# Kernel tuning notes

Hardware: AMD Instinct MI355X
Metric: run time of the kernel (lower is better)

Reference implementation:

```python
import jax, jax.numpy as jnp
import numpy as np

B, T, E, H = 512, 256, 384, 64

def setup_inputs() -> dict:
    key = jax.random.key(0)
    k1, k2, k3, k4 = jax.random.split(key, 4)
    scale = 1.0 / np.sqrt(E)
    return {
        "x":  jax.random.normal(k1, (B, T, E), dtype=jnp.float32),
        "Wq": jax.random.normal(k2, (E, H), dtype=jnp.float32) * scale,
        "Wk": jax.random.normal(k3, (E, H), dtype=jnp.float32) * scale,
        "Wv": jax.random.normal(k4, (E, H), dtype=jnp.float32) * scale,
    }

def reference(x, Wq, Wk, Wv):
    # single-head causal self-attention (dropout in eval mode / identity)
    q = jnp.einsum('bte,eh->bth', x, Wq)
    k = jnp.einsum('bte,eh->bth', x, Wk)
    v = jnp.einsum('bte,eh->bth', x, Wv)
    d = q.shape[-1]
    wei = jnp.einsum('bqh,bkh->bqk', q, k) * (d ** -0.5)   # [B,T,T]
    T_ = x.shape[1]
    causal = jnp.tril(jnp.ones((T_, T_), dtype=bool))
    wei = jnp.where(causal[None, :, :], wei, -jnp.inf)
    wei = jax.nn.softmax(wei, axis=-1)
    out = jnp.einsum('bqk,bkh->bqh', wei, v)               # [B,T,H]
    return out
```

## Files before the change

### kernel.cpp

```cpp
#include <hip/hip_runtime.h>

typedef __attribute__((ext_vector_type(4)))  float f32x4;
typedef __attribute__((ext_vector_type(16))) float f32x16;
typedef __attribute__((ext_vector_type(8)))  short s16x8;
typedef __attribute__((ext_vector_type(4)))  short s16x4;


__device__ inline short f2bf(float f){
  unsigned u = __float_as_uint(f);
  u = u + 0x7fffu + ((u >> 16) & 1u);
  return (short)(u >> 16);
}

__global__ void wt_prep_kernel(const float* __restrict__ Wq, const float* __restrict__ Wk,
                               const float* __restrict__ Wv, short* __restrict__ Wt){
  int o = blockIdx.x * 256 + threadIdx.x;
  if (o >= 192*384) return;
  int n = o / 384, k = o - n*384;
  const float* W = (n < 64) ? Wq : (n < 128) ? Wk : Wv;
  Wt[o] = f2bf(W[k*64 + (n & 63)]);
}

__global__ __launch_bounds__(512, 2) void fused_kernel(const float* __restrict__ x,
                             const short* __restrict__ Wt, float* __restrict__ out){
  __shared__ __align__(16) short Qs[256*72];
  __shared__ __align__(16) short Ks[256*72];
  __shared__ __align__(16) short Vts[64*264];
  __shared__ __align__(16) short Pp[8][16*40];

  const int tid  = threadIdx.x;
  const int w    = tid >> 6, lane = tid & 63;
  const int l31  = lane & 31, hh = lane >> 5;
  const int b    = blockIdx.x;

  const float* xb = x + ((long)b*256 + w*32)*384;

  f32x16 acc[6];
  #pragma unroll
  for (int c = 0; c < 6; ++c)
    #pragma unroll
    for (int j = 0; j < 16; ++j) acc[c][j] = 0.0f;

  #pragma unroll 2
  for (int kt = 0; kt < 6; ++kt){
    #pragma unroll
    for (int s = 0; s < 4; ++s){
      const int k0 = kt*64 + s*16 + hh*8;
      const float* xp = xb + l31*384 + k0;
      float4 a0 = *(const float4*)xp;
      float4 a1 = *(const float4*)(xp + 4);
      s16x8 bx;
      bx[0]=f2bf(a0.x); bx[1]=f2bf(a0.y); bx[2]=f2bf(a0.z); bx[3]=f2bf(a0.w);
      bx[4]=f2bf(a1.x); bx[5]=f2bf(a1.y); bx[6]=f2bf(a1.z); bx[7]=f2bf(a1.w);
      #pragma unroll
      for (int c = 0; c < 6; ++c){
        s16x8 wa = *(const s16x8*)(Wt + (c*32 + l31)*384 + k0);
        acc[c] = __builtin_amdgcn_mfma_f32_32x32x16_bf16(wa, bx, acc[c], 0, 0, 0);
      }
    }
  }

  const int trow = w*32 + l31;
  #pragma unroll
  for (int c = 0; c < 4; ++c){
    short* dst = (c < 2) ? Qs : Ks;
    const int nb = (c & 1)*32;
    #pragma unroll
    for (int g = 0; g < 4; ++g){
      s16x4 v;
      #pragma unroll
      for (int i = 0; i < 4; ++i) v[i] = f2bf(acc[c][g*4 + i]);
      *(s16x4*)(dst + trow*72 + nb + 8*g + 4*hh) = v;
    }
  }
  #pragma unroll
  for (int c = 4; c < 6; ++c)
    #pragma unroll
    for (int reg = 0; reg < 16; ++reg){
      const int h = (c-4)*32 + (reg & 3) + 8*(reg >> 2) + 4*hh;
      Vts[h*264 + trow] = f2bf(acc[c][reg]);
    }

  __syncthreads();

  const int l15 = lane & 15, quad = lane >> 4;
  float* ob = out + (long)b*256*64;
  short* Pw = Pp[w];

  for (int it = 0; it < 2; ++it){
    const int F  = it ? (15 - w) : w;
    const int qb = F*16;
    const int NF = F + 1;
    const int NS = (NF + 1) >> 1;

    s16x8 qf0 = *(const s16x8*)(Qs + (qb + l15)*72 + quad*8);
    s16x8 qf1 = *(const s16x8*)(Qs + (qb + l15)*72 + 32 + quad*8);

    f32x4 sc[16];
    #pragma unroll
    for (int f = 0; f < 16; ++f){
      f32x4 a;
      #pragma unroll
      for (int r = 0; r < 4; ++r) a[r] = 0.0f;
      if (f < NF){
        const short* kp = Ks + (f*16 + l15)*72 + quad*8;
        s16x8 k0v = *(const s16x8*)kp;
        s16x8 k1v = *(const s16x8*)(kp + 32);
        a = __builtin_amdgcn_mfma_f32_16x16x32_bf16(qf0, k0v, a, 0, 0, 0);
        a = __builtin_amdgcn_mfma_f32_16x16x32_bf16(qf1, k1v, a, 0, 0, 0);
      }
      sc[f] = a;
    }

    float mx[4], sm[4];
    #pragma unroll
    for (int r = 0; r < 4; ++r) mx[r] = -3.0e38f;
    #pragma unroll
    for (int f = 0; f < 16; ++f){
      if (f < NF){
        const int key = f*16 + l15;
        #pragma unroll
        for (int r = 0; r < 4; ++r){
          const int qg = qb + quad*4 + r;
          float s = sc[f][r] * 0.125f;
          s = (key <= qg) ? s : -1.0e30f;
          sc[f][r] = s;
          mx[r] = fmaxf(mx[r], s);
        }
      }
    }
    #pragma unroll
    for (int r = 0; r < 4; ++r){
      #pragma unroll
      for (int off = 1; off < 16; off <<= 1) mx[r] = fmaxf(mx[r], __shfl_xor(mx[r], off, 16));
    }
    #pragma unroll
    for (int r = 0; r < 4; ++r) sm[r] = 0.0f;
    #pragma unroll
    for (int f = 0; f < 16; ++f){
      if (f < NF){
        #pragma unroll
        for (int r = 0; r < 4; ++r){
          float p = exp2f((sc[f][r] - mx[r]) * 1.44269504f);
          sc[f][r] = p;
          sm[r] += p;
        }
      }
    }
    #pragma unroll
    for (int r = 0; r < 4; ++r){
      #pragma unroll
      for (int off = 1; off < 16; off <<= 1) sm[r] += __shfl_xor(sm[r], off, 16);
    }

    f32x4 o[4];
    #pragma unroll
    for (int h0 = 0; h0 < 4; ++h0)
      #pragma unroll
      for (int r = 0; r < 4; ++r) o[h0][r] = 0.0f;

    #pragma unroll
    for (int ks = 0; ks < 8; ++ks){
      if (ks < NS){
        #pragma unroll
        for (int fi = 0; fi < 2; ++fi){
          const int f = 2*ks + fi;
          #pragma unroll
          for (int r = 0; r < 4; ++r){
            short v = 0;
            if (f < NF) v = f2bf(sc[f][r]);
            Pw[(quad*4 + r)*40 + fi*16 + l15] = v;
          }
        }
        s16x8 pf = *(const s16x8*)(Pw + l15*40 + quad*8);
        #pragma unroll
        for (int h0 = 0; h0 < 4; ++h0){
          s16x8 vf = *(const s16x8*)(Vts + (h0*16 + l15)*264 + ks*32 + quad*8);
          o[h0] = __builtin_amdgcn_mfma_f32_16x16x32_bf16(pf, vf, o[h0], 0, 0, 0);
        }
      }
    }

    #pragma unroll
    for (int r = 0; r < 4; ++r){
      const float inv = 1.0f / sm[r];
      #pragma unroll
      for (int h0 = 0; h0 < 4; ++h0)
        ob[(qb + quad*4 + r)*64 + h0*16 + l15] = o[h0][r] * inv;
    }
  }
}

extern "C" void kernel_launch(void* const* d_in, const int* in_sizes, int n_in,
                              void* d_out, int out_size, void* d_ws, size_t ws_size,
                              hipStream_t stream){
  const float* x  = (const float*)d_in[0];
  const float* Wq = (const float*)d_in[1];
  const float* Wk = (const float*)d_in[2];
  const float* Wv = (const float*)d_in[3];
  float* out = (float*)d_out;

  short* Wt = (short*)d_ws;

  hipLaunchKernelGGL(wt_prep_kernel, dim3(288), dim3(256), 0, stream, Wq, Wk, Wv, Wt);
  hipLaunchKernelGGL(fused_kernel,   dim3(512), dim3(512), 0, stream, x, Wt, out);
}
```

Measured before the change: 363.0 us.

## Split fused attention into QKV projection and attention kernels via workspace

Replaces the single fused kernel with two kernels when the workspace is large enough. A QKV projection kernel writes bf16 Q, K and V^T to global memory with XOR-swizzled layouts, and an attention kernel loads K and V into LDS with global_load_lds and runs the causal softmax. The split lowers LDS and register pressure so each kernel can target 4 blocks per CU instead of 2. In exchange it adds about 48MB of global round-trip traffic and a second launch, and falls back to the fused kernel when the workspace is small.

```diff
diff --git a/kernel.cpp b/kernel.cpp
--- a/kernel.cpp
+++ b/kernel.cpp
@@ -10,6 +10,11 @@
   unsigned u = __float_as_uint(f);
   u = u + 0x7fffu + ((u >> 16) & 1u);
   return (short)(u >> 16);
+}
+
+__device__ __forceinline__ void gld16(const void* g, void* l){
+  __builtin_amdgcn_global_load_lds((const __attribute__((address_space(1))) void*)g,
+                                   (__attribute__((address_space(3))) void*)l, 16, 0, 0);
 }
 
 __global__ void wt_prep_kernel(const float* __restrict__ Wq, const float* __restrict__ Wk,
@@ -21,12 +26,229 @@
   Wt[o] = f2bf(W[k*64 + (n & 63)]);
 }
 
+__global__ __launch_bounds__(512, 4) void qkv_kernel(const float* __restrict__ x,
+    const short* __restrict__ Wt, short* __restrict__ Qg,
+    short* __restrict__ Kg, short* __restrict__ Vg){
+  const int tid  = threadIdx.x;
+  const int w    = tid >> 6, lane = tid & 63;
+  const int l15  = lane & 15, quad = lane >> 4;
+  const int b    = blockIdx.x;
+
+  const float* xb = x + (long)b*256*384;
+  short* Qb = Qg + (long)b*16384;
+  char*  Kb = (char*)(Kg + (long)b*16384);
+  char*  Vb = (char*)(Vg + (long)b*16384);
+
+  #pragma unroll 1
+  for (int p = 0; p < 2; ++p){
+    const int r0 = w*32 + p*16;
+    const int tr = r0 + l15;
+
+    f32x4 aq[4], ak[4], av[4];
+    #pragma unroll
+    for (int c = 0; c < 4; ++c)
+      #pragma unroll
+      for (int i = 0; i < 4; ++i){ aq[c][i]=0.f; ak[c][i]=0.f; av[c][i]=0.f; }
+
+    const float* xr = xb + (long)tr*384;
+    #pragma unroll 2
+    for (int kt = 0; kt < 12; ++kt){
+      const int k0 = kt*32 + quad*8;
+      float4 a0 = *(const float4*)(xr + k0);
+      float4 a1 = *(const float4*)(xr + k0 + 4);
+      s16x8 bx;
+      bx[0]=f2bf(a0.x); bx[1]=f2bf(a0.y); bx[2]=f2bf(a0.z); bx[3]=f2bf(a0.w);
+      bx[4]=f2bf(a1.x); bx[5]=f2bf(a1.y); bx[6]=f2bf(a1.z); bx[7]=f2bf(a1.w);
+      #pragma unroll
+      for (int c = 0; c < 4; ++c){
+        s16x8 wq = *(const s16x8*)(Wt + (c*16 + l15)*384 + k0);
+        aq[c] = __builtin_amdgcn_mfma_f32_16x16x32_bf16(wq, bx, aq[c], 0, 0, 0);
+      }
+      #pragma unroll
+      for (int c = 0; c < 4; ++c){
+        s16x8 wk = *(const s16x8*)(Wt + ((c+4)*16 + l15)*384 + k0);
+        ak[c] = __builtin_amdgcn_mfma_f32_16x16x32_bf16(wk, bx, ak[c], 0, 0, 0);
+      }
+      #pragma unroll
+      for (int c = 0; c < 4; ++c){
+        s16x8 wv = *(const s16x8*)(Wt + ((c+8)*16 + l15)*384 + k0);
+        av[c] = __builtin_amdgcn_mfma_f32_16x16x32_bf16(bx, wv, av[c], 0, 0, 0);
+      }
+    }
+
+    #pragma unroll
+    for (int c = 0; c < 4; ++c){
+      s16x4 v;
+      #pragma unroll
+      for (int i = 0; i < 4; ++i) v[i] = f2bf(aq[c][i]);
+      *(s16x4*)(Qb + tr*64 + c*16 + quad*4) = v;
+    }
+    {
+      const int swz = (tr & 7) << 4;
+      #pragma unroll
+      for (int c = 0; c < 4; ++c){
+        s16x4 v;
+        #pragma unroll
+        for (int i = 0; i < 4; ++i) v[i] = f2bf(ak[c][i]);
+        *(s16x4*)(Kb + tr*128 + ((c*32 + quad*8) ^ swz)) = v;
+      }
+    }
+    #pragma unroll
+    for (int c = 0; c < 4; ++c){
+      const int h   = c*16 + l15;
+      const int swz = (h & 7) << 4;
+      s16x4 v;
+      #pragma unroll
+      for (int i = 0; i < 4; ++i) v[i] = f2bf(av[c][i]);
+      *(s16x4*)(Vb + h*512 + (((r0 + quad*4)*2) ^ swz)) = v;
+    }
+  }
+}
+
+__global__ __launch_bounds__(512, 4) void attn_kernel(const short* __restrict__ Qg,
+    const short* __restrict__ Kg, const short* __restrict__ Vg,
+    float* __restrict__ out){
+  __shared__ __align__(16) short Ks[16384];
+  __shared__ __align__(16) short Vts[16384];
+  __shared__ __align__(16) short Pp[8][16*40];
+
+  const int tid  = threadIdx.x;
+  const int w    = tid >> 6, lane = tid & 63;
+  const int l15  = lane & 15, quad = lane >> 4;
+  const int b    = blockIdx.x;
+
+  const short* Qb = Qg + (long)b*16384;
+  const int F0 = w, F1 = 15 - w;
+  s16x8 qA0 = *(const s16x8*)(Qb + (F0*16 + l15)*64 + quad*8);
+  s16x8 qA1 = *(const s16x8*)(Qb + (F0*16 + l15)*64 + 32 + quad*8);
+  s16x8 qB0 = *(const s16x8*)(Qb + (F1*16 + l15)*64 + quad*8);
+  s16x8 qB1 = *(const s16x8*)(Qb + (F1*16 + l15)*64 + 32 + quad*8);
+
+  const char* Kb = (const char*)(Kg + (long)b*16384);
+  const char* Vb = (const char*)(Vg + (long)b*16384);
+  {
+    const int base = w*4096;
+    #pragma unroll
+    for (int i = 0; i < 4; ++i){
+      gld16(Kb + base + i*1024 + lane*16, (char*)Ks  + base + i*1024);
+      gld16(Vb + base + i*1024 + lane*16, (char*)Vts + base + i*1024);
+    }
+  }
+  __syncthreads();
+
+  float* ob = out + (long)b*256*64;
+  short* Pw = Pp[w];
+  const int swz = (l15 & 7) << 4;
+
+  auto attend = [&](int F, s16x8 qf0, s16x8 qf1){
+    const int qb = F*16;
+    const int NF = F + 1;
+    const int NS = (NF + 1) >> 1;
+
+    f32x4 sc[16];
+    #pragma unroll
+    for (int f = 0; f < 16; ++f){
+      f32x4 a;
+      #pragma unroll
+      for (int r = 0; r < 4; ++r) a[r] = 0.0f;
+      if (f < NF){
+        const char* kp = (const char*)Ks + (f*16 + l15)*128;
+        s16x8 k0v = *(const s16x8*)(kp + ((quad*16)      ^ swz));
+        s16x8 k1v = *(const s16x8*)(kp + ((64 + quad*16) ^ swz));
+        a = __builtin_amdgcn_mfma_f32_16x16x32_bf16(qf0, k0v, a, 0, 0, 0);
+        a = __builtin_amdgcn_mfma_f32_16x16x32_bf16(qf1, k1v, a, 0, 0, 0);
+      }
+      sc[f] = a;
+    }
+
+    float mx[4], sm[4];
+    #pragma unroll
+    for (int r = 0; r < 4; ++r) mx[r] = -3.0e38f;
+    #pragma unroll
+    for (int f = 0; f < 16; ++f){
+      if (f < NF){
+        const int key = f*16 + l15;
+        #pragma unroll
+        for (int r = 0; r < 4; ++r){
+          const int qg = qb + quad*4 + r;
+          float s = sc[f][r] * 0.125f;
+          s = (key <= qg) ? s : -1.0e30f;
+          sc[f][r] = s;
+          mx[r] = fmaxf(mx[r], s);
+        }
+      }
+    }
+    #pragma unroll
+    for (int r = 0; r < 4; ++r){
+      #pragma unroll
+      for (int off = 1; off < 16; off <<= 1) mx[r] = fmaxf(mx[r], __shfl_xor(mx[r], off, 16));
+    }
+    #pragma unroll
+    for (int r = 0; r < 4; ++r) sm[r] = 0.0f;
+    #pragma unroll
+    for (int f = 0; f < 16; ++f){
+      if (f < NF){
+        #pragma unroll
+        for (int r = 0; r < 4; ++r){
+          float p = exp2f((sc[f][r] - mx[r]) * 1.44269504f);
+          sc[f][r] = p;
+          sm[r] += p;
+        }
+      }
+    }
+    #pragma unroll
+    for (int r = 0; r < 4; ++r){
+      #pragma unroll
+      for (int off = 1; off < 16; off <<= 1) sm[r] += __shfl_xor(sm[r], off, 16);
+    }
+
+    f32x4 o[4];
+    #pragma unroll
+    for (int h0 = 0; h0 < 4; ++h0)
+      #pragma unroll
+      for (int r = 0; r < 4; ++r) o[h0][r] = 0.0f;
+
+    #pragma unroll
+    for (int ks = 0; ks < 8; ++ks){
+      if (ks < NS){
+        #pragma unroll
+        for (int fi = 0; fi < 2; ++fi){
+          const int f = 2*ks + fi;
+          #pragma unroll
+          for (int r = 0; r < 4; ++r){
+            short v = 0;
+            if (f < NF) v = f2bf(sc[f][r]);
+            Pw[(quad*4 + r)*40 + fi*16 + l15] = v;
+          }
+        }
+        s16x8 pf = *(const s16x8*)(Pw + l15*40 + quad*8);
+        #pragma unroll
+        for (int h0 = 0; h0 < 4; ++h0){
+          const char* vp = (const char*)Vts + (h0*16 + l15)*512;
+          s16x8 vf = *(const s16x8*)(vp + ((ks*64 + quad*16) ^ swz));
+          o[h0] = __builtin_amdgcn_mfma_f32_16x16x32_bf16(pf, vf, o[h0], 0, 0, 0);
+        }
+      }
+    }
+
+    #pragma unroll
+    for (int r = 0; r < 4; ++r){
+      const float inv = 1.0f / sm[r];
+      #pragma unroll
+      for (int h0 = 0; h0 < 4; ++h0)
+        ob[(qb + quad*4 + r)*64 + h0*16 + l15] = o[h0][r] * inv;
+    }
+  };
+  attend(F0, qA0, qA1);
+  attend(F1, qB0, qB1);
+}
+
 __global__ __launch_bounds__(512, 2) void fused_kernel(const float* __restrict__ x,
                              const short* __restrict__ Wt, float* __restrict__ out){
   __shared__ __align__(16) short Qs[256*72];
-  __shared__ __align__(16) short Ks[256*72];
-  __shared__ __align__(16) short Vts[64*264];
-  __shared__ __align__(16) short Pp[8][16*40];
+  __shared__ __align__(16) short Ks2[256*72];
+  __shared__ __align__(16) short Vts2[64*264];
+  __shared__ __align__(16) short Pp2[8][16*40];
 
   const int tid  = threadIdx.x;
   const int w    = tid >> 6, lane = tid & 63;
@@ -63,7 +285,7 @@
   const int trow = w*32 + l31;
   #pragma unroll
   for (int c = 0; c < 4; ++c){
-    short* dst = (c < 2) ? Qs : Ks;
+    short* dst = (c < 2) ? Qs : Ks2;
     const int nb = (c & 1)*32;
     #pragma unroll
     for (int g = 0; g < 4; ++g){
@@ -78,14 +300,14 @@
     #pragma unroll
     for (int reg = 0; reg < 16; ++reg){
       const int h = (c-4)*32 + (reg & 3) + 8*(reg >> 2) + 4*hh;
-      Vts[h*264 + trow] = f2bf(acc[c][reg]);
+      Vts2[h*264 + trow] = f2bf(acc[c][reg]);
     }
 
   __syncthreads();
 
   const int l15 = lane & 15, quad = lane >> 4;
   float* ob = out + (long)b*256*64;
-  short* Pw = Pp[w];
+  short* Pw = Pp2[w];
 
   for (int it = 0; it < 2; ++it){
     const int F  = it ? (15 - w) : w;
@@ -103,7 +325,7 @@
       #pragma unroll
       for (int r = 0; r < 4; ++r) a[r] = 0.0f;
       if (f < NF){
-        const short* kp = Ks + (f*16 + l15)*72 + quad*8;
+        const short* kp = Ks2 + (f*16 + l15)*72 + quad*8;
         s16x8 k0v = *(const s16x8*)kp;
         s16x8 k1v = *(const s16x8*)(kp + 32);
         a = __builtin_amdgcn_mfma_f32_16x16x32_bf16(qf0, k0v, a, 0, 0, 0);
@@ -175,7 +397,7 @@
         s16x8 pf = *(const s16x8*)(Pw + l15*40 + quad*8);
         #pragma unroll
         for (int h0 = 0; h0 < 4; ++h0){
-          s16x8 vf = *(const s16x8*)(Vts + (h0*16 + l15)*264 + ks*32 + quad*8);
+          s16x8 vf = *(const s16x8*)(Vts2 + (h0*16 + l15)*264 + ks*32 + quad*8);
           o[h0] = __builtin_amdgcn_mfma_f32_16x16x32_bf16(pf, vf, o[h0], 0, 0, 0);
         }
       }
@@ -201,7 +423,16 @@
   float* out = (float*)d_out;
 
   short* Wt = (short*)d_ws;
+  const size_t need = 147456 + 3ull*16777216ull;
 
   hipLaunchKernelGGL(wt_prep_kernel, dim3(288), dim3(256), 0, stream, Wq, Wk, Wv, Wt);
-  hipLaunchKernelGGL(fused_kernel,   dim3(512), dim3(512), 0, stream, x, Wt, out);
-}
+  if (ws_size >= need){
+    short* Qg = (short*)((char*)d_ws + 147456);
+    short* Kg = Qg + 8388608;
+    short* Vg = Kg + 8388608;
+    hipLaunchKernelGGL(qkv_kernel,  dim3(512), dim3(512), 0, stream, x, Wt, Qg, Kg, Vg);
+    hipLaunchKernelGGL(attn_kernel, dim3(512), dim3(512), 0, stream, Qg, Kg, Vg, out);
+  } else {
+    hipLaunchKernelGGL(fused_kernel, dim3(512), dim3(512), 0, stream, x, Wt, out);
+  }
+}
```

After: 424.1 us. 16.8% more time.

## Project QKV per query tile with 16x16 MFMA, keep Q in registers, swizzle LDS

Applied to the files above, without the earlier changes.

The QKV projection now runs with 16x16x32 MFMAs per 16-row tile, and each wave projects exactly the two query tiles it later attends. Q is staged through the K buffer row and kept in registers, so the Q shared array is gone. K and transposed V use XOR-swizzled unpadded layouts instead of padded ones. Together these cut LDS use and accumulator registers so launch bounds can ask for 4 blocks per CU. The cost is smaller MFMA tiles and more reloads of the weight fragments.

```diff
diff --git a/kernel.cpp b/kernel.cpp
--- a/kernel.cpp
+++ b/kernel.cpp
@@ -1,7 +1,6 @@
 #include <hip/hip_runtime.h>
 
 typedef __attribute__((ext_vector_type(4)))  float f32x4;
-typedef __attribute__((ext_vector_type(16))) float f32x16;
 typedef __attribute__((ext_vector_type(8)))  short s16x8;
 typedef __attribute__((ext_vector_type(4)))  short s16x4;
 
@@ -21,81 +20,101 @@
   Wt[o] = f2bf(W[k*64 + (n & 63)]);
 }
 
-__global__ __launch_bounds__(512, 2) void fused_kernel(const float* __restrict__ x,
+__global__ __launch_bounds__(512, 4) void fused2_kernel(const float* __restrict__ x,
                              const short* __restrict__ Wt, float* __restrict__ out){
-  __shared__ __align__(16) short Qs[256*72];
-  __shared__ __align__(16) short Ks[256*72];
-  __shared__ __align__(16) short Vts[64*264];
+  __shared__ __align__(16) char  KsB[32768];
+  __shared__ __align__(16) char  VtsB[32768];
   __shared__ __align__(16) short Pp[8][16*40];
 
   const int tid  = threadIdx.x;
   const int w    = tid >> 6, lane = tid & 63;
-  const int l31  = lane & 31, hh = lane >> 5;
+  const int l15  = lane & 15, quad = lane >> 4;
   const int b    = blockIdx.x;
 
-  const float* xb = x + ((long)b*256 + w*32)*384;
-
-  f32x16 acc[6];
-  #pragma unroll
-  for (int c = 0; c < 6; ++c)
-    #pragma unroll
-    for (int j = 0; j < 16; ++j) acc[c][j] = 0.0f;
-
-  #pragma unroll 2
-  for (int kt = 0; kt < 6; ++kt){
-    #pragma unroll
-    for (int s = 0; s < 4; ++s){
-      const int k0 = kt*64 + s*16 + hh*8;
-      const float* xp = xb + l31*384 + k0;
-      float4 a0 = *(const float4*)xp;
-      float4 a1 = *(const float4*)(xp + 4);
+  const float* xb = x + (long)b*256*384;
+  const int F0 = w, F1 = 15 - w;
+
+  s16x8 qA0, qA1, qB0, qB1;
+
+  auto project = [&](int r0, s16x8& qf0, s16x8& qf1){
+    f32x4 aq[4], ak[4], av[4];
+    #pragma unroll
+    for (int c = 0; c < 4; ++c)
+      #pragma unroll
+      for (int i = 0; i < 4; ++i){ aq[c][i]=0.f; ak[c][i]=0.f; av[c][i]=0.f; }
+
+    const float* xr = xb + (long)(r0 + l15)*384;
+    #pragma unroll 2
+    for (int kt = 0; kt < 12; ++kt){
+      const int k0 = kt*32 + quad*8;
+      float4 a0 = *(const float4*)(xr + k0);
+      float4 a1 = *(const float4*)(xr + k0 + 4);
       s16x8 bx;
       bx[0]=f2bf(a0.x); bx[1]=f2bf(a0.y); bx[2]=f2bf(a0.z); bx[3]=f2bf(a0.w);
       bx[4]=f2bf(a1.x); bx[5]=f2bf(a1.y); bx[6]=f2bf(a1.z); bx[7]=f2bf(a1.w);
       #pragma unroll
-      for (int c = 0; c < 6; ++c){
-        s16x8 wa = *(const s16x8*)(Wt + (c*32 + l31)*384 + k0);
-        acc[c] = __builtin_amdgcn_mfma_f32_32x32x16_bf16(wa, bx, acc[c], 0, 0, 0);
-      }
-    }
-  }
-
-  const int trow = w*32 + l31;
-  #pragma unroll
-  for (int c = 0; c < 4; ++c){
-    short* dst = (c < 2) ? Qs : Ks;
-    const int nb = (c & 1)*32;
-    #pragma unroll
-    for (int g = 0; g < 4; ++g){
+      for (int c = 0; c < 4; ++c){
+        s16x8 wq = *(const s16x8*)(Wt + (c*16 + l15)*384 + k0);
+        aq[c] = __builtin_amdgcn_mfma_f32_16x16x32_bf16(wq, bx, aq[c], 0, 0, 0);
+      }
+      #pragma unroll
+      for (int c = 0; c < 4; ++c){
+        s16x8 wk = *(const s16x8*)(Wt + ((c+4)*16 + l15)*384 + k0);
+        ak[c] = __builtin_amdgcn_mfma_f32_16x16x32_bf16(wk, bx, ak[c], 0, 0, 0);
+      }
+      #pragma unroll
+      for (int c = 0; c < 4; ++c){
+        s16x8 wv = *(const s16x8*)(Wt + ((c+8)*16 + l15)*384 + k0);
+        av[c] = __builtin_amdgcn_mfma_f32_16x16x32_bf16(bx, wv, av[c], 0, 0, 0);
+      }
+    }
+
+    char* krow = KsB + (r0 + l15)*128;
+    const int swzr = (l15 & 7) << 4;
+
+    #pragma unroll
+    for (int c = 0; c < 4; ++c){
       s16x4 v;
       #pragma unroll
-      for (int i = 0; i < 4; ++i) v[i] = f2bf(acc[c][g*4 + i]);
-      *(s16x4*)(dst + trow*72 + nb + 8*g + 4*hh) = v;
-    }
-  }
-  #pragma unroll
-  for (int c = 4; c < 6; ++c)
-    #pragma unroll
-    for (int reg = 0; reg < 16; ++reg){
-      const int h = (c-4)*32 + (reg & 3) + 8*(reg >> 2) + 4*hh;
-      Vts[h*264 + trow] = f2bf(acc[c][reg]);
-    }
+      for (int i = 0; i < 4; ++i) v[i] = f2bf(aq[c][i]);
+      *(s16x4*)(krow + ((c*32 + quad*8) ^ swzr)) = v;
+    }
+    asm volatile("s_waitcnt lgkmcnt(0)" ::: "memory");
+    qf0 = *(const s16x8*)(krow + ((quad*16)      ^ swzr));
+    qf1 = *(const s16x8*)(krow + ((64 + quad*16) ^ swzr));
+    asm volatile("s_waitcnt lgkmcnt(0)" ::: "memory");
+
+    #pragma unroll
+    for (int c = 0; c < 4; ++c){
+      s16x4 v;
+      #pragma unroll
+      for (int i = 0; i < 4; ++i) v[i] = f2bf(ak[c][i]);
+      *(s16x4*)(krow + ((c*32 + quad*8) ^ swzr)) = v;
+    }
+    #pragma unroll
+    for (int c = 0; c < 4; ++c){
+      const int h = c*16 + l15;
+      s16x4 v;
+      #pragma unroll
+      for (int i = 0; i < 4; ++i) v[i] = f2bf(av[c][i]);
+      *(s16x4*)(VtsB + h*512 + (((r0 + quad*4)*2) ^ ((h & 7) << 4))) = v;
+    }
+  };
+
+  project(F0*16, qA0, qA1);
+  project(F1*16, qB0, qB1);
 
   __syncthreads();
 
-  const int l15 = lane & 15, quad = lane >> 4;
   float* ob = out + (long)b*256*64;
   short* Pw = Pp[w];
-
-  for (int it = 0; it < 2; ++it){
-    const int F  = it ? (15 - w) : w;
+  const int swz = (l15 & 7) << 4;
+
+  auto attend = [&](int F, s16x8 qf0, s16x8 qf1){
     const int qb = F*16;
     const int NF = F + 1;
     const int NS = (NF + 1) >> 1;
 
-    s16x8 qf0 = *(const s16x8*)(Qs + (qb + l15)*72 + quad*8);
-    s16x8 qf1 = *(const s16x8*)(Qs + (qb + l15)*72 + 32 + quad*8);
-
     f32x4 sc[16];
     #pragma unroll
     for (int f = 0; f < 16; ++f){
@@ -103,9 +122,9 @@
       #pragma unroll
       for (int r = 0; r < 4; ++r) a[r] = 0.0f;
       if (f < NF){
-        const short* kp = Ks + (f*16 + l15)*72 + quad*8;
-        s16x8 k0v = *(const s16x8*)kp;
-        s16x8 k1v = *(const s16x8*)(kp + 32);
+        const char* kp = KsB + (f*16 + l15)*128;
+        s16x8 k0v = *(const s16x8*)(kp + ((quad*16)      ^ swz));
+        s16x8 k1v = *(const s16x8*)(kp + ((64 + quad*16) ^ swz));
         a = __builtin_amdgcn_mfma_f32_16x16x32_bf16(qf0, k0v, a, 0, 0, 0);
         a = __builtin_amdgcn_mfma_f32_16x16x32_bf16(qf1, k1v, a, 0, 0, 0);
       }
@@ -175,7 +194,8 @@
         s16x8 pf = *(const s16x8*)(Pw + l15*40 + quad*8);
         #pragma unroll
         for (int h0 = 0; h0 < 4; ++h0){
-          s16x8 vf = *(const s16x8*)(Vts + (h0*16 + l15)*264 + ks*32 + quad*8);
+          const char* vp = VtsB + (h0*16 + l15)*512;
+          s16x8 vf = *(const s16x8*)(vp + ((ks*64 + quad*16) ^ swz));
           o[h0] = __builtin_amdgcn_mfma_f32_16x16x32_bf16(pf, vf, o[h0], 0, 0, 0);
         }
       }
@@ -188,7 +208,10 @@
       for (int h0 = 0; h0 < 4; ++h0)
         ob[(qb + quad*4 + r)*64 + h0*16 + l15] = o[h0][r] * inv;
     }
-  }
+  };
+
+  attend(F0, qA0, qA1);
+  attend(F1, qB0, qB1);
 }
 
 extern "C" void kernel_launch(void* const* d_in, const int* in_sizes, int n_in,
@@ -203,5 +226,5 @@
   short* Wt = (short*)d_ws;
 
   hipLaunchKernelGGL(wt_prep_kernel, dim3(288), dim3(256), 0, stream, Wq, Wk, Wv, Wt);
-  hipLaunchKernelGGL(fused_kernel,   dim3(512), dim3(512), 0, stream, x, Wt, out);
-}
+  hipLaunchKernelGGL(fused2_kernel,  dim3(512), dim3(512), 0, stream, x, Wt, out);
+}
```

Result: slower. 396.1 us (+9.1%).
